# Kernel tuning notes

Hardware: AMD Instinct MI355X
Metric: run time of the kernel (lower is better)

The kernel has to match this reference:

```python
import jax, jax.numpy as jnp
import numpy as np

N = 262144          # flattened node batch
IN_S, IN_V = 256, 32
OUT_S, OUT_V = 256, 32
H = max(IN_V, OUT_V)  # 32
EPS = 1e-4


def setup_inputs() -> dict:
    key = jax.random.key(0)
    ks = jax.random.split(key, 8)
    inv = lambda f: 1.0 / np.sqrt(f).astype(np.float32)
    return {
        "s": jax.random.normal(ks[0], (N, IN_S), jnp.float32),
        "V": jax.random.normal(ks[1], (N, IN_V, 3), jnp.float32),
        "W_h": jax.random.normal(ks[2], (H, IN_V), jnp.float32) * inv(IN_V),
        "W_mu": jax.random.normal(ks[3], (OUT_V, H), jnp.float32) * inv(H),
        "W_m_w": jax.random.normal(ks[4], (OUT_S, H + IN_S), jnp.float32) * inv(H + IN_S),
        "W_m_b": jax.random.normal(ks[5], (OUT_S,), jnp.float32) * 0.01,
        "W_g_w": jax.random.normal(ks[6], (OUT_V, OUT_S), jnp.float32) * inv(OUT_S),
        "W_g_b": jax.random.normal(ks[7], (OUT_V,), jnp.float32) * 0.01,
    }


def reference(s, V, W_h, W_mu, W_m_w, W_m_b, W_g_w, W_g_b):
    # V_h = W_h @ V : [N, H, 3]
    V_h = jnp.einsum('hv,nvc->nhc', W_h, V)
    # per-row L2 norm, clipped at eps : [N, H]
    s_h = jnp.maximum(jnp.linalg.norm(V_h, axis=-1), EPS)
    # Linear on concatenated scalars : [N, OUT_S]
    s_m = jnp.concatenate([s, s_h], axis=-1) @ W_m_w.T + W_m_b
    s_dash = jax.nn.relu(s_m)                      # sigma = relu
    # V_mu = W_mu @ V_h : [N, OUT_V, 3]
    V_mu = jnp.einsum('mh,nhc->nmc', W_mu, V_h)
    # vector gate: sigmoid(W_g(sigmoid(s_m)))  (sigma_plus = sigmoid)
    gate = jax.nn.sigmoid(jax.nn.sigmoid(s_m) @ W_g_w.T + W_g_b)  # [N, OUT_V]
    V_dash = gate[..., None] * V_mu
    return s_dash, V_dash
```

## Files before the change

kernel.cpp:

```cpp
#include <hip/hip_runtime.h>

#define NTOT 262144
#define BN   32
#define NT   256
#define SXS  296
#define VTS  36

typedef __attribute__((ext_vector_type(8))) short bf16x8;
typedef __attribute__((ext_vector_type(4))) float f32x4;

static __device__ __forceinline__ unsigned pk2(float lo, float hi) {
    unsigned r;
    asm("v_cvt_pk_bf16_f32 %0, %1, %2" : "=v"(r) : "v"(lo), "v"(hi));
    return r;
}
static __device__ __forceinline__ unsigned short f2b(float x) {
    union { float f; unsigned u; } c; c.f = x;
    unsigned r = c.u + 0x7FFFu + ((c.u >> 16) & 1u);
    return (unsigned short)(r >> 16);
}
static __device__ __forceinline__ float b2f(unsigned short h) {
    union { unsigned u; float f; } c; c.u = ((unsigned)h) << 16; return c.f;
}
static __device__ __forceinline__ bf16x8 cvt8(const float* p) {
    float4 x = *(const float4*)p, y = *(const float4*)(p + 4);
    union { unsigned u[4]; bf16x8 v; } r;
    r.u[0] = pk2(x.x, x.y); r.u[1] = pk2(x.z, x.w);
    r.u[2] = pk2(y.x, y.y); r.u[3] = pk2(y.z, y.w);
    return r.v;
}
static __device__ __forceinline__ void glds16(const unsigned short* g, void* l) {
    __builtin_amdgcn_global_load_lds(
        (const __attribute__((address_space(1))) void*)g,
        (__attribute__((address_space(3))) void*)l, 16, 0, 0);
}

__global__ void pack_w(const float* __restrict__ Wmw, const float* __restrict__ Wgw,
                       unsigned short* __restrict__ wp) {
    int t = blockIdx.x * 256 + threadIdx.x;
    if (t < 73728) {
        int o = t / 288, k = t % 288;
        int ks = k >> 5, kk = k & 31, ch = o >> 7, ol = o & 127;
        int kks = kk ^ (((ol >> 1) & 3) << 3);
        wp[(ks * 2 + ch) * 4096 + ol * 32 + kks] = (unsigned short)pk2(Wmw[t], Wmw[t]);
    } else if (t < 81920) {
        int j = t - 73728;
        int o = j >> 8, k = j & 255;
        wp[73728 + (k >> 5) * 1024 + o * 32 + (k & 31)] = (unsigned short)pk2(Wgw[j], Wgw[j]);
    }
}

template<int USE_WS>
__global__ __launch_bounds__(NT, 3)
void gvp_main(const float* __restrict__ s, const float* __restrict__ V,
              const float* __restrict__ Wh, const float* __restrict__ Wmu,
              const float* __restrict__ Wmw, const float* __restrict__ Wmb,
              const float* __restrict__ Wgw, const float* __restrict__ Wgb,
              const unsigned short* __restrict__ wpack,
              float* __restrict__ out)
{
    __shared__ __attribute__((aligned(16))) unsigned short sX[BN * SXS];
    __shared__ __attribute__((aligned(16))) unsigned short sWb[2 * 4096];
    __shared__ __attribute__((aligned(16))) unsigned short sVT[96 * VTS];

    const int t  = threadIdx.x;
    const int w  = t >> 6, l = t & 63;
    const int fr = l & 15, fq = l >> 4;
    const int n0 = blockIdx.x * BN;
    const int half = w & 1, oh = w >> 1;

    if (USE_WS) {
        #pragma unroll
        for (int c = 0; c < 2; ++c) {
            const unsigned short* src = wpack + c * 4096 + w * 1024 + l * 8;
            unsigned short* dst = sWb + c * 4096 + w * 1024;
            glds16(src, dst);
            glds16(src + 512, dst + 512);
        }
    }

    #pragma unroll
    for (int i = 0; i < 8; ++i) {
        int n = i * 4 + w;
        float4 x4 = *(const float4*)&s[(size_t)(n0 + n) * 256 + 4 * l];
        uint2 h2 = { pk2(x4.x, x4.y), pk2(x4.z, x4.w) };
        *(uint2*)&sX[n * SXS + 4 * l] = h2;
    }
    {
        int n = t >> 3, vq = t & 7;
        const float* p = &V[(size_t)(n0 + n) * 96 + vq * 12];
        float4 q0 = *(const float4*)(p);
        float4 q1 = *(const float4*)(p + 4);
        float4 q2 = *(const float4*)(p + 8);
        uint2 c0 = { pk2(q0.x, q0.w), pk2(q1.z, q2.y) };
        uint2 c1 = { pk2(q0.y, q1.x), pk2(q1.w, q2.z) };
        uint2 c2 = { pk2(q0.z, q1.y), pk2(q2.x, q2.w) };
        *(uint2*)&sVT[(0 * 32 + n) * VTS + vq * 4] = c0;
        *(uint2*)&sVT[(1 * 32 + n) * VTS + vq * 4] = c1;
        *(uint2*)&sVT[(2 * 32 + n) * VTS + vq * 4] = c2;
    }
    if (!USE_WS) {
        #pragma unroll
        for (int c = 0; c < 2; ++c) {
            int ol = w * 32 + (l >> 1), kh = l & 1, x = (ol >> 1) & 3;
            const float* p = &Wmw[(c * 128 + ol) * 288 + kh * 16];
            unsigned short* dst = sWb + c * 4096;
            *(bf16x8*)&dst[ol * 32 + (((kh * 2 + 0) ^ x) << 3)] = cvt8(p);
            *(bf16x8*)&dst[ol * 32 + (((kh * 2 + 1) ^ x) << 3)] = cvt8(p + 8);
        }
    }
    __syncthreads();

    {
        bf16x8 bh = cvt8(&Wh[(oh * 16 + fr) * 32 + fq * 8]);
        f32x4 va0 = {0,0,0,0}, va1 = {0,0,0,0}, va2 = {0,0,0,0};
        bf16x8 a0 = *(const bf16x8*)&sVT[(0 * 32 + half * 16 + fr) * VTS + fq * 8];
        bf16x8 a1 = *(const bf16x8*)&sVT[(1 * 32 + half * 16 + fr) * VTS + fq * 8];
        bf16x8 a2 = *(const bf16x8*)&sVT[(2 * 32 + half * 16 + fr) * VTS + fq * 8];
        va0 = __builtin_amdgcn_mfma_f32_16x16x32_bf16(a0, bh, va0, 0, 0, 0);
        va1 = __builtin_amdgcn_mfma_f32_16x16x32_bf16(a1, bh, va1, 0, 0, 0);
        va2 = __builtin_amdgcn_mfma_f32_16x16x32_bf16(a2, bh, va2, 0, 0, 0);
        __syncthreads();
        #pragma unroll
        for (int r = 0; r < 4; ++r) {
            int nl = half * 16 + fq * 4 + r;
            int h  = oh * 16 + fr;
            sVT[(0 * 32 + nl) * VTS + h] = f2b(va0[r]);
            sVT[(1 * 32 + nl) * VTS + h] = f2b(va1[r]);
            sVT[(2 * 32 + nl) * VTS + h] = f2b(va2[r]);
            float nrm = sqrtf(fmaf(va0[r], va0[r], fmaf(va1[r], va1[r], va2[r] * va2[r])));
            sX[nl * SXS + 256 + h] = f2b(fmaxf(nrm, 1e-4f));
        }
    }
    __syncthreads();

    f32x4 acc[2][4];
    #pragma unroll
    for (int mt = 0; mt < 2; ++mt)
        #pragma unroll
        for (int j = 0; j < 4; ++j) acc[mt][j] = (f32x4){0.f, 0.f, 0.f, 0.f};

    const int ol0 = w * 32 + fr, ol1 = ol0 + 16;
    const int bo0 = ol0 * 32 + ((fq ^ ((ol0 >> 1) & 3)) << 3);
    const int bo1 = ol1 * 32 + ((fq ^ ((ol1 >> 1) & 3)) << 3);

    #pragma unroll
    for (int it = 0; it < 18; ++it) {
        if (it >= 2) {
            if (it <= 16) asm volatile("s_waitcnt vmcnt(2)" ::: "memory");
            else          asm volatile("s_waitcnt vmcnt(0)" ::: "memory");
            __builtin_amdgcn_sched_barrier(0);
        }
        const int ks = it >> 1;
        const unsigned short* bw = sWb + (it & 1) * 4096;
        bf16x8 a0 = *(const bf16x8*)&sX[fr * SXS + ks * 32 + fq * 8];
        bf16x8 a1 = *(const bf16x8*)&sX[(16 + fr) * SXS + ks * 32 + fq * 8];
        bf16x8 b0 = *(const bf16x8*)&bw[bo0];
        bf16x8 b1v = *(const bf16x8*)&bw[bo1];
        if (it < 16) {
            asm volatile("s_waitcnt lgkmcnt(0)" ::: "memory");
            __builtin_amdgcn_sched_barrier(0);
            if (USE_WS) {
                const unsigned short* src = wpack + (it + 2) * 4096 + w * 1024 + l * 8;
                unsigned short* dst = sWb + (it & 1) * 4096 + w * 1024;
                glds16(src, dst);
                glds16(src + 512, dst + 512);
            } else {
                int it2 = it + 2, ks2 = it2 >> 1, ch2 = it2 & 1;
                int ol = w * 32 + (l >> 1), kh = l & 1, x = (ol >> 1) & 3;
                const float* p = &Wmw[(ch2 * 128 + ol) * 288 + ks2 * 32 + kh * 16];
                unsigned short* dst = sWb + (it & 1) * 4096;
                *(bf16x8*)&dst[ol * 32 + (((kh * 2 + 0) ^ x) << 3)] = cvt8(p);
                *(bf16x8*)&dst[ol * 32 + (((kh * 2 + 1) ^ x) << 3)] = cvt8(p + 8);
            }
        }
        const int ji = (it & 1) * 2;
        acc[0][ji + 0] = __builtin_amdgcn_mfma_f32_16x16x32_bf16(a0, b0, acc[0][ji + 0], 0, 0, 0);
        acc[1][ji + 0] = __builtin_amdgcn_mfma_f32_16x16x32_bf16(a1, b0, acc[1][ji + 0], 0, 0, 0);
        acc[0][ji + 1] = __builtin_amdgcn_mfma_f32_16x16x32_bf16(a0, b1v, acc[0][ji + 1], 0, 0, 0);
        acc[1][ji + 1] = __builtin_amdgcn_mfma_f32_16x16x32_bf16(a1, b1v, acc[1][ji + 1], 0, 0, 0);
    }
    __syncthreads();

    float bias[4];
    #pragma unroll
    for (int ji = 0; ji < 4; ++ji)
        bias[ji] = Wmb[(ji >> 1) * 128 + w * 32 + (ji & 1) * 16 + fr];

    const int skw = ((fq & 1) << 4) | ((fq >> 1) << 3);
    float* sRel = (float*)sWb;
    #pragma unroll
    for (int mt = 0; mt < 2; ++mt) {
        #pragma unroll
        for (int r = 0; r < 4; ++r) {
            int row  = fq * 4 + r;
            int node = mt * 16 + row;
            #pragma unroll
            for (int ji = 0; ji < 4; ++ji) {
                int col = (ji >> 1) * 128 + w * 32 + (ji & 1) * 16 + fr;
                float m = acc[mt][ji][r] + bias[ji];
                sX[node * SXS + col] = f2b(1.f / (1.f + __expf(-m)));
                sRel[row * 256 + (col ^ skw)] = fmaxf(m, 0.f);
            }
        }
        __syncthreads();
        #pragma unroll
        for (int i = 0; i < 4; ++i) {
            int flat = i * NT + t;
            int row = flat >> 6, c4 = flat & 63;
            int sk2 = (((row >> 2) & 1) << 4) | (((row >> 3) & 1) << 3);
            float4 v4 = *(const float4*)&sRel[row * 256 + ((c4 * 4) ^ sk2)];
            *(float4*)&out[(size_t)(n0 + mt * 16 + row) * 256 + c4 * 4] = v4;
        }
        __syncthreads();
    }

    {
        const int gmt = w & 1, gnt = w >> 1;
        f32x4 g = (f32x4){0.f, 0.f, 0.f, 0.f};
        #pragma unroll
        for (int ks = 0; ks < 8; ++ks) {
            bf16x8 a = *(const bf16x8*)&sX[(gmt * 16 + fr) * SXS + ks * 32 + fq * 8];
            bf16x8 b;
            if (USE_WS) b = *(const bf16x8*)&wpack[73728 + ks * 1024 + (gnt * 16 + fr) * 32 + fq * 8];
            else        b = cvt8(&Wgw[(gnt * 16 + fr) * 256 + ks * 32 + fq * 8]);
            g = __builtin_amdgcn_mfma_f32_16x16x32_bf16(a, b, g, 0, 0, 0);
        }
        int mo = gnt * 16 + fr;
        float gb = Wgb[mo];
        #pragma unroll
        for (int r = 0; r < 4; ++r) {
            int node = gmt * 16 + fq * 4 + r;
            sX[node * SXS + 256 + mo] = f2b(1.f / (1.f + __expf(-(g[r] + gb))));
        }
    }
    __syncthreads();

    float* sc = (float*)sWb;
    {
        bf16x8 bm = cvt8(&Wmu[(oh * 16 + fr) * 32 + fq * 8]);
        f32x4 m0 = {0,0,0,0}, m1 = {0,0,0,0}, m2 = {0,0,0,0};
        bf16x8 a0 = *(const bf16x8*)&sVT[(0 * 32 + half * 16 + fr) * VTS + fq * 8];
        bf16x8 a1 = *(const bf16x8*)&sVT[(1 * 32 + half * 16 + fr) * VTS + fq * 8];
        bf16x8 a2 = *(const bf16x8*)&sVT[(2 * 32 + half * 16 + fr) * VTS + fq * 8];
        m0 = __builtin_amdgcn_mfma_f32_16x16x32_bf16(a0, bm, m0, 0, 0, 0);
        m1 = __builtin_amdgcn_mfma_f32_16x16x32_bf16(a1, bm, m1, 0, 0, 0);
        m2 = __builtin_amdgcn_mfma_f32_16x16x32_bf16(a2, bm, m2, 0, 0, 0);
        #pragma unroll
        for (int r = 0; r < 4; ++r) {
            int node = half * 16 + fq * 4 + r;
            int m    = oh * 16 + fr;
            float g  = b2f(sX[node * SXS + 256 + m]);
            sc[node * 96 + m * 3 + 0] = g * m0[r];
            sc[node * 96 + m * 3 + 1] = g * m1[r];
            sc[node * 96 + m * 3 + 2] = g * m2[r];
        }
    }
    __syncthreads();
    const size_t VBASE = (size_t)NTOT * 256;
    #pragma unroll
    for (int i = 0; i < 3; ++i) {
        int f = i * NT + t;
        *(float4*)&out[VBASE + (size_t)n0 * 96 + f * 4] = *(const float4*)&sc[f * 4];
    }
}

extern "C" void kernel_launch(void* const* d_in, const int* in_sizes, int n_in,
                              void* d_out, int out_size, void* d_ws, size_t ws_size,
                              hipStream_t stream) {
    const float* s   = (const float*)d_in[0];
    const float* V   = (const float*)d_in[1];
    const float* Wh  = (const float*)d_in[2];
    const float* Wmu = (const float*)d_in[3];
    const float* Wmw = (const float*)d_in[4];
    const float* Wmb = (const float*)d_in[5];
    const float* Wgw = (const float*)d_in[6];
    const float* Wgb = (const float*)d_in[7];
    float* out = (float*)d_out;

    dim3 grid(NTOT / BN);
    dim3 block(NT);

    if (ws_size >= 163840) {
        pack_w<<<320, 256, 0, stream>>>(Wmw, Wgw, (unsigned short*)d_ws);
        gvp_main<1><<<grid, block, 0, stream>>>(s, V, Wh, Wmu, Wmw, Wmb, Wgw, Wgb,
                                                (const unsigned short*)d_ws, out);
    } else {
        gvp_main<0><<<grid, block, 0, stream>>>(s, V, Wh, Wmu, Wmw, Wmb, Wgw, Wgb,
                                                nullptr, out);
    }
}
```

Measured before the change: 208.7 us.

## Process two node tiles per block with register prefetch of next tile inputs

Each block now handles two consecutive 32-node tiles and halves the grid. The second tile's s and V loads are issued into registers after the first tile's main GEMM, so they overlap the epilogue and stores. This aims to hide global load latency, at the cost of extra live registers, possible spills under the launch bound, and fewer blocks in flight.

After: 252.3 us. 1.21x slower.

```diff
diff --git a/kernel.cpp b/kernel.cpp
--- a/kernel.cpp
+++ b/kernel.cpp
@@ -66,202 +66,227 @@
     const int t  = threadIdx.x;
     const int w  = t >> 6, l = t & 63;
     const int fr = l & 15, fq = l >> 4;
-    const int n0 = blockIdx.x * BN;
     const int half = w & 1, oh = w >> 1;
 
-    if (USE_WS) {
-        #pragma unroll
-        for (int c = 0; c < 2; ++c) {
-            const unsigned short* src = wpack + c * 4096 + w * 1024 + l * 8;
-            unsigned short* dst = sWb + c * 4096 + w * 1024;
-            glds16(src, dst);
-            glds16(src + 512, dst + 512);
-        }
-    }
+    float4 pfs[8];
+    float4 pfv0, pfv1, pfv2;
 
     #pragma unroll
-    for (int i = 0; i < 8; ++i) {
-        int n = i * 4 + w;
-        float4 x4 = *(const float4*)&s[(size_t)(n0 + n) * 256 + 4 * l];
-        uint2 h2 = { pk2(x4.x, x4.y), pk2(x4.z, x4.w) };
-        *(uint2*)&sX[n * SXS + 4 * l] = h2;
-    }
-    {
-        int n = t >> 3, vq = t & 7;
-        const float* p = &V[(size_t)(n0 + n) * 96 + vq * 12];
-        float4 q0 = *(const float4*)(p);
-        float4 q1 = *(const float4*)(p + 4);
-        float4 q2 = *(const float4*)(p + 8);
-        uint2 c0 = { pk2(q0.x, q0.w), pk2(q1.z, q2.y) };
-        uint2 c1 = { pk2(q0.y, q1.x), pk2(q1.w, q2.z) };
-        uint2 c2 = { pk2(q0.z, q1.y), pk2(q2.x, q2.w) };
-        *(uint2*)&sVT[(0 * 32 + n) * VTS + vq * 4] = c0;
-        *(uint2*)&sVT[(1 * 32 + n) * VTS + vq * 4] = c1;
-        *(uint2*)&sVT[(2 * 32 + n) * VTS + vq * 4] = c2;
-    }
-    if (!USE_WS) {
-        #pragma unroll
-        for (int c = 0; c < 2; ++c) {
-            int ol = w * 32 + (l >> 1), kh = l & 1, x = (ol >> 1) & 3;
-            const float* p = &Wmw[(c * 128 + ol) * 288 + kh * 16];
-            unsigned short* dst = sWb + c * 4096;
-            *(bf16x8*)&dst[ol * 32 + (((kh * 2 + 0) ^ x) << 3)] = cvt8(p);
-            *(bf16x8*)&dst[ol * 32 + (((kh * 2 + 1) ^ x) << 3)] = cvt8(p + 8);
-        }
-    }
-    __syncthreads();
-
-    {
-        bf16x8 bh = cvt8(&Wh[(oh * 16 + fr) * 32 + fq * 8]);
-        f32x4 va0 = {0,0,0,0}, va1 = {0,0,0,0}, va2 = {0,0,0,0};
-        bf16x8 a0 = *(const bf16x8*)&sVT[(0 * 32 + half * 16 + fr) * VTS + fq * 8];
-        bf16x8 a1 = *(const bf16x8*)&sVT[(1 * 32 + half * 16 + fr) * VTS + fq * 8];
-        bf16x8 a2 = *(const bf16x8*)&sVT[(2 * 32 + half * 16 + fr) * VTS + fq * 8];
-        va0 = __builtin_amdgcn_mfma_f32_16x16x32_bf16(a0, bh, va0, 0, 0, 0);
-        va1 = __builtin_amdgcn_mfma_f32_16x16x32_bf16(a1, bh, va1, 0, 0, 0);
-        va2 = __builtin_amdgcn_mfma_f32_16x16x32_bf16(a2, bh, va2, 0, 0, 0);
-        __syncthreads();
-        #pragma unroll
-        for (int r = 0; r < 4; ++r) {
-            int nl = half * 16 + fq * 4 + r;
-            int h  = oh * 16 + fr;
-            sVT[(0 * 32 + nl) * VTS + h] = f2b(va0[r]);
-            sVT[(1 * 32 + nl) * VTS + h] = f2b(va1[r]);
-            sVT[(2 * 32 + nl) * VTS + h] = f2b(va2[r]);
-            float nrm = sqrtf(fmaf(va0[r], va0[r], fmaf(va1[r], va1[r], va2[r] * va2[r])));
-            sX[nl * SXS + 256 + h] = f2b(fmaxf(nrm, 1e-4f));
-        }
-    }
-    __syncthreads();
-
-    f32x4 acc[2][4];
-    #pragma unroll
-    for (int mt = 0; mt < 2; ++mt)
-        #pragma unroll
-        for (int j = 0; j < 4; ++j) acc[mt][j] = (f32x4){0.f, 0.f, 0.f, 0.f};
-
-    const int ol0 = w * 32 + fr, ol1 = ol0 + 16;
-    const int bo0 = ol0 * 32 + ((fq ^ ((ol0 >> 1) & 3)) << 3);
-    const int bo1 = ol1 * 32 + ((fq ^ ((ol1 >> 1) & 3)) << 3);
-
-    #pragma unroll
-    for (int it = 0; it < 18; ++it) {
-        if (it >= 2) {
-            if (it <= 16) asm volatile("s_waitcnt vmcnt(2)" ::: "memory");
-            else          asm volatile("s_waitcnt vmcnt(0)" ::: "memory");
-            __builtin_amdgcn_sched_barrier(0);
-        }
-        const int ks = it >> 1;
-        const unsigned short* bw = sWb + (it & 1) * 4096;
-        bf16x8 a0 = *(const bf16x8*)&sX[fr * SXS + ks * 32 + fq * 8];
-        bf16x8 a1 = *(const bf16x8*)&sX[(16 + fr) * SXS + ks * 32 + fq * 8];
-        bf16x8 b0 = *(const bf16x8*)&bw[bo0];
-        bf16x8 b1v = *(const bf16x8*)&bw[bo1];
-        if (it < 16) {
-            asm volatile("s_waitcnt lgkmcnt(0)" ::: "memory");
-            __builtin_amdgcn_sched_barrier(0);
-            if (USE_WS) {
-                const unsigned short* src = wpack + (it + 2) * 4096 + w * 1024 + l * 8;
-                unsigned short* dst = sWb + (it & 1) * 4096 + w * 1024;
+    for (int tt = 0; tt < 2; ++tt) {
+        const int n0 = (blockIdx.x * 2 + tt) * BN;
+
+        if (USE_WS) {
+            #pragma unroll
+            for (int c = 0; c < 2; ++c) {
+                const unsigned short* src = wpack + c * 4096 + w * 1024 + l * 8;
+                unsigned short* dst = sWb + c * 4096 + w * 1024;
                 glds16(src, dst);
                 glds16(src + 512, dst + 512);
-            } else {
-                int it2 = it + 2, ks2 = it2 >> 1, ch2 = it2 & 1;
+            }
+        }
+
+        #pragma unroll
+        for (int i = 0; i < 8; ++i) {
+            int n = i * 4 + w;
+            float4 x4 = (tt == 0)
+                ? *(const float4*)&s[(size_t)(n0 + n) * 256 + 4 * l]
+                : pfs[i];
+            uint2 h2 = { pk2(x4.x, x4.y), pk2(x4.z, x4.w) };
+            *(uint2*)&sX[n * SXS + 4 * l] = h2;
+        }
+        {
+            int n = t >> 3, vq = t & 7;
+            float4 q0, q1, q2;
+            if (tt == 0) {
+                const float* p = &V[(size_t)(n0 + n) * 96 + vq * 12];
+                q0 = *(const float4*)(p);
+                q1 = *(const float4*)(p + 4);
+                q2 = *(const float4*)(p + 8);
+            } else { q0 = pfv0; q1 = pfv1; q2 = pfv2; }
+            uint2 c0 = { pk2(q0.x, q0.w), pk2(q1.z, q2.y) };
+            uint2 c1 = { pk2(q0.y, q1.x), pk2(q1.w, q2.z) };
+            uint2 c2 = { pk2(q0.z, q1.y), pk2(q2.x, q2.w) };
+            *(uint2*)&sVT[(0 * 32 + n) * VTS + vq * 4] = c0;
+            *(uint2*)&sVT[(1 * 32 + n) * VTS + vq * 4] = c1;
+            *(uint2*)&sVT[(2 * 32 + n) * VTS + vq * 4] = c2;
+        }
+        if (!USE_WS) {
+            #pragma unroll
+            for (int c = 0; c < 2; ++c) {
                 int ol = w * 32 + (l >> 1), kh = l & 1, x = (ol >> 1) & 3;
-                const float* p = &Wmw[(ch2 * 128 + ol) * 288 + ks2 * 32 + kh * 16];
-                unsigned short* dst = sWb + (it & 1) * 4096;
+                const float* p = &Wmw[(c * 128 + ol) * 288 + kh * 16];
+                unsigned short* dst = sWb + c * 4096;
                 *(bf16x8*)&dst[ol * 32 + (((kh * 2 + 0) ^ x) << 3)] = cvt8(p);
                 *(bf16x8*)&dst[ol * 32 + (((kh * 2 + 1) ^ x) << 3)] = cvt8(p + 8);
             }
         }
-        const int ji = (it & 1) * 2;
-        acc[0][ji + 0] = __builtin_amdgcn_mfma_f32_16x16x32_bf16(a0, b0, acc[0][ji + 0], 0, 0, 0);
-        acc[1][ji + 0] = __builtin_amdgcn_mfma_f32_16x16x32_bf16(a1, b0, acc[1][ji + 0], 0, 0, 0);
-        acc[0][ji + 1] = __builtin_amdgcn_mfma_f32_16x16x32_bf16(a0, b1v, acc[0][ji + 1], 0, 0, 0);
-        acc[1][ji + 1] = __builtin_amdgcn_mfma_f32_16x16x32_bf16(a1, b1v, acc[1][ji + 1], 0, 0, 0);
-    }
-    __syncthreads();
-
-    float bias[4];
-    #pragma unroll
-    for (int ji = 0; ji < 4; ++ji)
-        bias[ji] = Wmb[(ji >> 1) * 128 + w * 32 + (ji & 1) * 16 + fr];
-
-    const int skw = ((fq & 1) << 4) | ((fq >> 1) << 3);
-    float* sRel = (float*)sWb;
-    #pragma unroll
-    for (int mt = 0; mt < 2; ++mt) {
-        #pragma unroll
-        for (int r = 0; r < 4; ++r) {
-            int row  = fq * 4 + r;
-            int node = mt * 16 + row;
-            #pragma unroll
-            for (int ji = 0; ji < 4; ++ji) {
-                int col = (ji >> 1) * 128 + w * 32 + (ji & 1) * 16 + fr;
-                float m = acc[mt][ji][r] + bias[ji];
-                sX[node * SXS + col] = f2b(1.f / (1.f + __expf(-m)));
-                sRel[row * 256 + (col ^ skw)] = fmaxf(m, 0.f);
-            }
-        }
-        __syncthreads();
-        #pragma unroll
-        for (int i = 0; i < 4; ++i) {
-            int flat = i * NT + t;
-            int row = flat >> 6, c4 = flat & 63;
-            int sk2 = (((row >> 2) & 1) << 4) | (((row >> 3) & 1) << 3);
-            float4 v4 = *(const float4*)&sRel[row * 256 + ((c4 * 4) ^ sk2)];
-            *(float4*)&out[(size_t)(n0 + mt * 16 + row) * 256 + c4 * 4] = v4;
-        }
-        __syncthreads();
-    }
-
-    {
-        const int gmt = w & 1, gnt = w >> 1;
-        f32x4 g = (f32x4){0.f, 0.f, 0.f, 0.f};
-        #pragma unroll
-        for (int ks = 0; ks < 8; ++ks) {
-            bf16x8 a = *(const bf16x8*)&sX[(gmt * 16 + fr) * SXS + ks * 32 + fq * 8];
-            bf16x8 b;
-            if (USE_WS) b = *(const bf16x8*)&wpack[73728 + ks * 1024 + (gnt * 16 + fr) * 32 + fq * 8];
-            else        b = cvt8(&Wgw[(gnt * 16 + fr) * 256 + ks * 32 + fq * 8]);
-            g = __builtin_amdgcn_mfma_f32_16x16x32_bf16(a, b, g, 0, 0, 0);
-        }
-        int mo = gnt * 16 + fr;
-        float gb = Wgb[mo];
-        #pragma unroll
-        for (int r = 0; r < 4; ++r) {
-            int node = gmt * 16 + fq * 4 + r;
-            sX[node * SXS + 256 + mo] = f2b(1.f / (1.f + __expf(-(g[r] + gb))));
-        }
-    }
-    __syncthreads();
-
-    float* sc = (float*)sWb;
-    {
-        bf16x8 bm = cvt8(&Wmu[(oh * 16 + fr) * 32 + fq * 8]);
-        f32x4 m0 = {0,0,0,0}, m1 = {0,0,0,0}, m2 = {0,0,0,0};
-        bf16x8 a0 = *(const bf16x8*)&sVT[(0 * 32 + half * 16 + fr) * VTS + fq * 8];
-        bf16x8 a1 = *(const bf16x8*)&sVT[(1 * 32 + half * 16 + fr) * VTS + fq * 8];
-        bf16x8 a2 = *(const bf16x8*)&sVT[(2 * 32 + half * 16 + fr) * VTS + fq * 8];
-        m0 = __builtin_amdgcn_mfma_f32_16x16x32_bf16(a0, bm, m0, 0, 0, 0);
-        m1 = __builtin_amdgcn_mfma_f32_16x16x32_bf16(a1, bm, m1, 0, 0, 0);
-        m2 = __builtin_amdgcn_mfma_f32_16x16x32_bf16(a2, bm, m2, 0, 0, 0);
-        #pragma unroll
-        for (int r = 0; r < 4; ++r) {
-            int node = half * 16 + fq * 4 + r;
-            int m    = oh * 16 + fr;
-            float g  = b2f(sX[node * SXS + 256 + m]);
-            sc[node * 96 + m * 3 + 0] = g * m0[r];
-            sc[node * 96 + m * 3 + 1] = g * m1[r];
-            sc[node * 96 + m * 3 + 2] = g * m2[r];
-        }
-    }
-    __syncthreads();
-    const size_t VBASE = (size_t)NTOT * 256;
-    #pragma unroll
-    for (int i = 0; i < 3; ++i) {
-        int f = i * NT + t;
-        *(float4*)&out[VBASE + (size_t)n0 * 96 + f * 4] = *(const float4*)&sc[f * 4];
+        __syncthreads();
+
+        {
+            bf16x8 bh = cvt8(&Wh[(oh * 16 + fr) * 32 + fq * 8]);
+            f32x4 va0 = {0,0,0,0}, va1 = {0,0,0,0}, va2 = {0,0,0,0};
+            bf16x8 a0 = *(const bf16x8*)&sVT[(0 * 32 + half * 16 + fr) * VTS + fq * 8];
+            bf16x8 a1 = *(const bf16x8*)&sVT[(1 * 32 + half * 16 + fr) * VTS + fq * 8];
+            bf16x8 a2 = *(const bf16x8*)&sVT[(2 * 32 + half * 16 + fr) * VTS + fq * 8];
+            va0 = __builtin_amdgcn_mfma_f32_16x16x32_bf16(a0, bh, va0, 0, 0, 0);
+            va1 = __builtin_amdgcn_mfma_f32_16x16x32_bf16(a1, bh, va1, 0, 0, 0);
+            va2 = __builtin_amdgcn_mfma_f32_16x16x32_bf16(a2, bh, va2, 0, 0, 0);
+            __syncthreads();
+            #pragma unroll
+            for (int r = 0; r < 4; ++r) {
+                int nl = half * 16 + fq * 4 + r;
+                int h  = oh * 16 + fr;
+                sVT[(0 * 32 + nl) * VTS + h] = f2b(va0[r]);
+                sVT[(1 * 32 + nl) * VTS + h] = f2b(va1[r]);
+                sVT[(2 * 32 + nl) * VTS + h] = f2b(va2[r]);
+                float nrm = sqrtf(fmaf(va0[r], va0[r], fmaf(va1[r], va1[r], va2[r] * va2[r])));
+                sX[nl * SXS + 256 + h] = f2b(fmaxf(nrm, 1e-4f));
+            }
+        }
+        __syncthreads();
+
+        f32x4 acc[2][4];
+        #pragma unroll
+        for (int mt = 0; mt < 2; ++mt)
+            #pragma unroll
+            for (int j = 0; j < 4; ++j) acc[mt][j] = (f32x4){0.f, 0.f, 0.f, 0.f};
+
+        const int ol0 = w * 32 + fr, ol1 = ol0 + 16;
+        const int bo0 = ol0 * 32 + ((fq ^ ((ol0 >> 1) & 3)) << 3);
+        const int bo1 = ol1 * 32 + ((fq ^ ((ol1 >> 1) & 3)) << 3);
+
+        #pragma unroll
+        for (int it = 0; it < 18; ++it) {
+            if (it >= 2) {
+                if (it <= 16) asm volatile("s_waitcnt vmcnt(2)" ::: "memory");
+                else          asm volatile("s_waitcnt vmcnt(0)" ::: "memory");
+                __builtin_amdgcn_sched_barrier(0);
+            }
+            const int ks = it >> 1;
+            const unsigned short* bw = sWb + (it & 1) * 4096;
+            bf16x8 a0 = *(const bf16x8*)&sX[fr * SXS + ks * 32 + fq * 8];
+            bf16x8 a1 = *(const bf16x8*)&sX[(16 + fr) * SXS + ks * 32 + fq * 8];
+            bf16x8 b0 = *(const bf16x8*)&bw[bo0];
+            bf16x8 b1v = *(const bf16x8*)&bw[bo1];
+            if (it < 16) {
+                asm volatile("s_waitcnt lgkmcnt(0)" ::: "memory");
+                __builtin_amdgcn_sched_barrier(0);
+                if (USE_WS) {
+                    const unsigned short* src = wpack + (it + 2) * 4096 + w * 1024 + l * 8;
+                    unsigned short* dst = sWb + (it & 1) * 4096 + w * 1024;
+                    glds16(src, dst);
+                    glds16(src + 512, dst + 512);
+                } else {
+                    int it2 = it + 2, ks2 = it2 >> 1, ch2 = it2 & 1;
+                    int ol = w * 32 + (l >> 1), kh = l & 1, x = (ol >> 1) & 3;
+                    const float* p = &Wmw[(ch2 * 128 + ol) * 288 + ks2 * 32 + kh * 16];
+                    unsigned short* dst = sWb + (it & 1) * 4096;
+                    *(bf16x8*)&dst[ol * 32 + (((kh * 2 + 0) ^ x) << 3)] = cvt8(p);
+                    *(bf16x8*)&dst[ol * 32 + (((kh * 2 + 1) ^ x) << 3)] = cvt8(p + 8);
+                }
+            }
+            const int ji = (it & 1) * 2;
+            acc[0][ji + 0] = __builtin_amdgcn_mfma_f32_16x16x32_bf16(a0, b0, acc[0][ji + 0], 0, 0, 0);
+            acc[1][ji + 0] = __builtin_amdgcn_mfma_f32_16x16x32_bf16(a1, b0, acc[1][ji + 0], 0, 0, 0);
+            acc[0][ji + 1] = __builtin_amdgcn_mfma_f32_16x16x32_bf16(a0, b1v, acc[0][ji + 1], 0, 0, 0);
+            acc[1][ji + 1] = __builtin_amdgcn_mfma_f32_16x16x32_bf16(a1, b1v, acc[1][ji + 1], 0, 0, 0);
+        }
+        __syncthreads();
+
+        if (tt == 0) {
+            const int n1 = n0 + BN;
+            #pragma unroll
+            for (int i = 0; i < 8; ++i)
+                pfs[i] = *(const float4*)&s[(size_t)(n1 + i * 4 + w) * 256 + 4 * l];
+            int n = t >> 3, vq = t & 7;
+            const float* p = &V[(size_t)(n1 + n) * 96 + vq * 12];
+            pfv0 = *(const float4*)(p);
+            pfv1 = *(const float4*)(p + 4);
+            pfv2 = *(const float4*)(p + 8);
+        }
+
+        float bias[4];
+        #pragma unroll
+        for (int ji = 0; ji < 4; ++ji)
+            bias[ji] = Wmb[(ji >> 1) * 128 + w * 32 + (ji & 1) * 16 + fr];
+
+        const int skw = ((fq & 1) << 4) | ((fq >> 1) << 3);
+        float* sRel = (float*)sWb;
+        #pragma unroll
+        for (int mt = 0; mt < 2; ++mt) {
+            #pragma unroll
+            for (int r = 0; r < 4; ++r) {
+                int row  = fq * 4 + r;
+                int node = mt * 16 + row;
+                #pragma unroll
+                for (int ji = 0; ji < 4; ++ji) {
+                    int col = (ji >> 1) * 128 + w * 32 + (ji & 1) * 16 + fr;
+                    float m = acc[mt][ji][r] + bias[ji];
+                    sX[node * SXS + col] = f2b(1.f / (1.f + __expf(-m)));
+                    sRel[row * 256 + (col ^ skw)] = fmaxf(m, 0.f);
+                }
+            }
+            __syncthreads();
+            #pragma unroll
+            for (int i = 0; i < 4; ++i) {
+                int flat = i * NT + t;
+                int row = flat >> 6, c4 = flat & 63;
+                int sk2 = (((row >> 2) & 1) << 4) | (((row >> 3) & 1) << 3);
+                float4 v4 = *(const float4*)&sRel[row * 256 + ((c4 * 4) ^ sk2)];
+                *(float4*)&out[(size_t)(n0 + mt * 16 + row) * 256 + c4 * 4] = v4;
+            }
+            __syncthreads();
+        }
+
+        {
+            const int gmt = w & 1, gnt = w >> 1;
+            f32x4 g = (f32x4){0.f, 0.f, 0.f, 0.f};
+            #pragma unroll
+            for (int ks = 0; ks < 8; ++ks) {
+                bf16x8 a = *(const bf16x8*)&sX[(gmt * 16 + fr) * SXS + ks * 32 + fq * 8];
+                bf16x8 b;
+                if (USE_WS) b = *(const bf16x8*)&wpack[73728 + ks * 1024 + (gnt * 16 + fr) * 32 + fq * 8];
+                else        b = cvt8(&Wgw[(gnt * 16 + fr) * 256 + ks * 32 + fq * 8]);
+                g = __builtin_amdgcn_mfma_f32_16x16x32_bf16(a, b, g, 0, 0, 0);
+            }
+            int mo = gnt * 16 + fr;
+            float gb = Wgb[mo];
+            #pragma unroll
+            for (int r = 0; r < 4; ++r) {
+                int node = gmt * 16 + fq * 4 + r;
+                sX[node * SXS + 256 + mo] = f2b(1.f / (1.f + __expf(-(g[r] + gb))));
+            }
+        }
+        __syncthreads();
+
+        float* sc = (float*)sWb;
+        {
+            bf16x8 bm = cvt8(&Wmu[(oh * 16 + fr) * 32 + fq * 8]);
+            f32x4 m0 = {0,0,0,0}, m1 = {0,0,0,0}, m2 = {0,0,0,0};
+            bf16x8 a0 = *(const bf16x8*)&sVT[(0 * 32 + half * 16 + fr) * VTS + fq * 8];
+            bf16x8 a1 = *(const bf16x8*)&sVT[(1 * 32 + half * 16 + fr) * VTS + fq * 8];
+            bf16x8 a2 = *(const bf16x8*)&sVT[(2 * 32 + half * 16 + fr) * VTS + fq * 8];
+            m0 = __builtin_amdgcn_mfma_f32_16x16x32_bf16(a0, bm, m0, 0, 0, 0);
+            m1 = __builtin_amdgcn_mfma_f32_16x16x32_bf16(a1, bm, m1, 0, 0, 0);
+            m2 = __builtin_amdgcn_mfma_f32_16x16x32_bf16(a2, bm, m2, 0, 0, 0);
+            #pragma unroll
+            for (int r = 0; r < 4; ++r) {
+                int node = half * 16 + fq * 4 + r;
+                int m    = oh * 16 + fr;
+                float g  = b2f(sX[node * SXS + 256 + m]);
+                sc[node * 96 + m * 3 + 0] = g * m0[r];
+                sc[node * 96 + m * 3 + 1] = g * m1[r];
+                sc[node * 96 + m * 3 + 2] = g * m2[r];
+            }
+        }
+        __syncthreads();
+        const size_t VBASE = (size_t)NTOT * 256;
+        #pragma unroll
+        for (int i = 0; i < 3; ++i) {
+            int f = i * NT + t;
+            *(float4*)&out[VBASE + (size_t)n0 * 96 + f * 4] = *(const float4*)&sc[f * 4];
+        }
+        __syncthreads();
     }
 }
 
@@ -278,7 +303,7 @@
     const float* Wgb = (const float*)d_in[7];
     float* out = (float*)d_out;
 
-    dim3 grid(NTOT / BN);
+    dim3 grid(NTOT / BN / 2);
     dim3 block(NT);
 
     if (ws_size >= 163840) {
```
